# Performance work log

Hardware: AMD Instinct MI355X
Metric: run time of the kernel (lower is better)

## Reference

```python
import jax, jax.numpy as jnp
import numpy as np
from jax import lax

INPUT_SIZE = 64
HIDDEN_SIZE = 4096
OUTPUT_SIZE = 16
SEQ_LEN = 4096
SPECTRAL_RADIUS = 0.95
LEAKY_RATE = 0.9
INPUT_SCALING = 1.0
FEEDBACK_SCALING = 0.1
SPARSITY = 0.1


def setup_inputs() -> dict:
    key = jax.random.key(0)
    ks = jax.random.split(key, 7)
    X = jax.random.normal(ks[0], (SEQ_LEN, INPUT_SIZE), dtype=jnp.float32)
    W_in = jax.random.normal(ks[1], (HIDDEN_SIZE, INPUT_SIZE), dtype=jnp.float32) * INPUT_SCALING
    # sparse reservoir matrix, scaled so spectral radius ~ SPECTRAL_RADIUS
    dense = jax.random.normal(ks[2], (HIDDEN_SIZE, HIDDEN_SIZE), dtype=jnp.float32)
    mask = (jax.random.uniform(ks[3], (HIDDEN_SIZE, HIDDEN_SIZE)) < SPARSITY).astype(jnp.float32)
    # circular-law estimate of spectral radius for sparse gaussian: sqrt(density*N)
    scale = SPECTRAL_RADIUS / np.sqrt(SPARSITY * HIDDEN_SIZE)
    W_res = dense * mask * scale
    b = jax.random.normal(ks[4], (HIDDEN_SIZE,), dtype=jnp.float32)
    W_fb = jax.random.normal(ks[5], (HIDDEN_SIZE, OUTPUT_SIZE), dtype=jnp.float32) * FEEDBACK_SCALING
    W_out = jax.random.normal(ks[6], (OUTPUT_SIZE, HIDDEN_SIZE), dtype=jnp.float32) * 0.01
    return {"X": X, "W_in": W_in, "W_res": W_res, "b": b, "W_fb": W_fb, "W_out": W_out}


def reference(X, W_in, W_res, b, W_fb, W_out):
    """ESN with feedback + leaky integration; Force readout (inference: y = W_out @ s).
    Returns (results [T, O], outputs [T, H]) matching ESNForce.forward."""
    H = W_res.shape[0]
    O = W_out.shape[0]

    def step(carry, x_t):
        s, y = carry  # previous state [H], previous output [O]
        pre = W_in @ x_t + W_res @ s + b + W_fb @ y
        s_new = (1.0 - LEAKY_RATE) * s + LEAKY_RATE * jnp.tanh(pre)
        y_new = W_out @ s_new
        return (s_new, y_new), (y_new, s_new)

    init = (jnp.zeros((H,), dtype=X.dtype), jnp.zeros((O,), dtype=X.dtype))
    _, (results, outputs) = lax.scan(step, init, X)
    return results, outputs
```

## Files before the change

### kernel.cpp

```cpp
#include <hip/hip_runtime.h>
#include <cstdint>

#define NBLK 128
#define BLOCK 1024
#define ROWS 32
#define HDIM 4096
#define IDIM 64
#define ODIM 16
#define TSTEPS 4096
#define PAD 576
#define GMAX 18
#define LEAK 0.9f
#define SU 11
#define SUS 12
#define YU 8

typedef float f32x4 __attribute__((ext_vector_type(4)));

__global__ void init_ws(float* ws) {
    int i = blockIdx.x * blockDim.x + threadIdx.x;
    if (i < (2 * NBLK * SUS + 2 * NBLK * YU) * 4) ws[i] = 0.0f;
}

__global__ __launch_bounds__(BLOCK) void esn_kernel(
    const float* __restrict__ X,
    const float* __restrict__ Win,
    const float* __restrict__ Wres,
    const float* __restrict__ bvec,
    const float* __restrict__ Wfb,
    const float* __restrict__ Wout,
    float* __restrict__ out,
    float* __restrict__ sx,
    float* __restrict__ yx)
{
    __shared__ float          ell_val[ROWS][PAD];
    __shared__ unsigned short ell_idx[ROWS][PAD];
    __shared__ __align__(16) float s_lds[2][HDIM];
    __shared__ float          win_lds[ROWS][IDIM];
    __shared__ float          wfb_lds[ROWS][ODIM];
    __shared__ __align__(8)  float wout_lds[ROWS][ODIM];
    __shared__ float          b_lds[ROWS];
    __shared__ float          x_lds[2][IDIM];
    __shared__ float          y_lds[2][ODIM];
    __shared__ __align__(16) float snew_lds[ROWS];
    __shared__ unsigned       snflag[ROWS];
    __shared__ int            nnz_lds[ROWS];
    __shared__ int            rnds_lds[ROWS];
    __shared__ unsigned char  bankCnt[ROWS][32];
    __shared__ unsigned char  grpCnt[ROWS][GMAX];

    const int tid   = threadIdx.x;
    const int blk   = blockIdx.x;
    const int rbase = blk * ROWS;
    const int rowB  = tid >> 5;
    const int lB    = tid & 31;
    const int wv    = tid >> 6;
    const int ln    = tid & 63;

    for (int i = tid; i < ROWS * PAD; i += BLOCK) {
        ell_val[i / PAD][i % PAD] = 0.0f;
        ell_idx[i / PAD][i % PAD] = 0;
    }
    for (int i = tid; i < ROWS * 32; i += BLOCK) bankCnt[i >> 5][i & 31] = 0;
    for (int i = tid; i < ROWS * GMAX; i += BLOCK) grpCnt[i / GMAX][i % GMAX] = 0;
    if (tid < ROWS) snflag[tid] = 0u;

    {
        for (int rr = wv * 2; rr < wv * 2 + 2; ++rr) {
            const float* wrow = Wres + (size_t)(rbase + rr) * HDIM;
            int cnt = 0;
            for (int c0 = 0; c0 < HDIM; c0 += 64)
                cnt += __popcll(__ballot(wrow[c0 + ln] != 0.0f));
            if (ln == 0) {
                int nz = cnt < PAD ? cnt : PAD;
                nnz_lds[rr] = nz;
                int gu = (nz + 31) >> 5;
                if (gu < 1) gu = 1;
                if (gu > GMAX) gu = GMAX;
                rnds_lds[rr] = (gu + 1) >> 1;
            }
        }
    }
    __syncthreads();

    {
        if (ln == 0 || ln == 32) {
            const int row = wv * 2 + (ln >> 5);
            const int nz  = nnz_lds[row];
            int gu = (nz + 31) >> 5;
            if (gu < 1) gu = 1;
            if (gu > GMAX) gu = GMAX;
            const float* wrow = Wres + (size_t)(rbase + row) * HDIM;
            int placed = 0;
            for (int c = 0; c < HDIM && placed < nz; ++c) {
                const float w = wrow[c];
                if (w != 0.0f) {
                    const int b = c & 31;
                    const int r = bankCnt[row][b];
                    bankCnt[row][b] = (unsigned char)(r + 1);
                    int g = r % gu;
                    int p = grpCnt[row][g];
                    int guard = 0;
                    while (p >= 32 && guard < GMAX) {
                        g = (g + 1 == gu) ? 0 : g + 1;
                        p = grpCnt[row][g];
                        ++guard;
                    }
                    if (p >= 32) break;
                    grpCnt[row][g] = (unsigned char)(p + 1);
                    const int slot = ((g >> 1) << 6) + 2 * p + (g & 1);
                    ell_val[row][slot] = w;
                    ell_idx[row][slot] = (unsigned short)c;
                    ++placed;
                }
            }
        }
    }

    for (int i = tid; i < ROWS * IDIM; i += BLOCK)
        win_lds[i >> 6][i & 63] = Win[(size_t)(rbase + (i >> 6)) * IDIM + (i & 63)];
    for (int i = tid; i < ROWS * ODIM; i += BLOCK)
        wfb_lds[i >> 4][i & 15] = Wfb[(size_t)(rbase + (i >> 4)) * ODIM + (i & 15)];
    for (int i = tid; i < ROWS * ODIM; i += BLOCK)
        wout_lds[i >> 4][i & 15] = Wout[(size_t)(i & 15) * HDIM + rbase + (i >> 4)];
    if (tid < ROWS) b_lds[tid] = bvec[rbase + tid];

    for (int i = tid; i < HDIM; i += BLOCK) s_lds[0][i] = 0.0f;
    if (tid < ODIM) y_lds[0][tid] = 0.0f;
    if (tid >= 64 && tid < 128) x_lds[0][tid - 64] = X[tid - 64];
    __syncthreads();

    float* out_res = out;
    float* out_s   = out + (size_t)TSTEPS * ODIM;
    const int RB = rnds_lds[rowB];

    for (int t = 0; t < TSTEPS; ++t) {
        const unsigned tu = (unsigned)(t + 1);
        const float tagf = __uint_as_float(tu);
        const int cur = t & 1, nxt = cur ^ 1;

        {
            const float* sc = s_lds[cur];
            float a0 = 0.0f, a1 = 0.0f;
            for (int k = 0; k < RB; ++k) {
                const int e = (k << 6) + (lB << 1);
                const float2  v  = *(const float2*)&ell_val[rowB][e];
                const ushort2 ix = *(const ushort2*)&ell_idx[rowB][e];
                a0 += v.x * sc[ix.x];
                a1 += v.y * sc[ix.y];
            }
            float acc = a0 + a1;
            acc += win_lds[rowB][lB] * x_lds[cur][lB]
                 + win_lds[rowB][lB + 32] * x_lds[cur][lB + 32];
            if (lB < ODIM) acc += wfb_lds[rowB][lB] * y_lds[cur][lB];
            acc += __shfl_xor(acc, 16, 32);
            acc += __shfl_xor(acc, 8, 32);
            acc += __shfl_xor(acc, 4, 32);
            acc += __shfl_xor(acc, 2, 32);
            acc += __shfl_xor(acc, 1, 32);
            if (lB == 0) {
                const float pre = acc + b_lds[rowB];
                snew_lds[rowB] = (1.0f - LEAK) * sc[rbase + rowB] + LEAK * tanhf(pre);
                __hip_atomic_store(&snflag[rowB], tu, __ATOMIC_RELEASE,
                                   __HIP_MEMORY_SCOPE_WORKGROUP);
            }
        }

        if (wv == 0) {
            for (;;) {
                unsigned f = (ln < ROWS)
                    ? __hip_atomic_load(&snflag[ln], __ATOMIC_ACQUIRE, __HIP_MEMORY_SCOPE_WORKGROUP)
                    : tu;
                if (__all(f >= tu)) break;
            }
            if (ln >= 16 && ln < 16 + SU) {
                const int j  = ln - 16;
                const int b0 = 3 * j;
                const int b1 = (3 * j + 1 < 32) ? 3 * j + 1 : 31;
                const int b2 = (3 * j + 2 < 32) ? 3 * j + 2 : 31;
                f32x4 v;
                v.x = snew_lds[b0]; v.y = snew_lds[b1]; v.z = snew_lds[b2]; v.w = tagf;
                float* dst = sx + (((size_t)cur * NBLK + blk) * SUS + j) * 4;
                asm volatile("global_store_dwordx4 %0, %1, off sc0 sc1"
                             :: "v"(dst), "v"(v) : "memory");
            }
            if (ln < YU) {
                float a0 = 0.0f, a1 = 0.0f;
                #pragma unroll
                for (int r = 0; r < ROWS; ++r) {
                    const float2 w = *(const float2*)&wout_lds[r][2 * ln];
                    a0 += w.x * snew_lds[r];
                    a1 += w.y * snew_lds[r];
                }
                f32x4 v; v.x = a0; v.y = a1; v.z = tagf; v.w = 0.0f;
                float* dst = yx + (((size_t)cur * NBLK + blk) * YU + ln) * 4;
                asm volatile("global_store_dwordx4 %0, %1, off sc0 sc1"
                             :: "v"(dst), "v"(v) : "memory");
            }
            if (ln >= 32 && ln < 40) {
                const int j = ln - 32;
                *(f32x4*)(out_s + (size_t)t * HDIM + rbase + j * 4) =
                    *(const f32x4*)&snew_lds[j * 4];
            }
        } else if (wv == 1) {
            if (t + 1 < TSTEPS) x_lds[nxt][ln] = X[(size_t)(t + 1) * IDIM + ln];
            const int u  = ln & 7;
            const int pg = ln >> 3;
            const float* yb = yx + (size_t)cur * NBLK * YU * 4;
            f32x4 w0,w1,w2,w3,w4,w5,w6,w7,w8,w9,w10,w11,w12,w13,w14,w15;
            for (;;) {
                #define YL(i) asm volatile("global_load_dwordx4 %0, %1, off sc0 sc1" \
                    : "=v"(w##i) : "v"(yb + (((pg << 4) + i) * YU + u) * 4));
                YL(0) YL(1) YL(2) YL(3) YL(4) YL(5) YL(6) YL(7)
                YL(8) YL(9) YL(10) YL(11) YL(12) YL(13) YL(14) YL(15)
                #undef YL
                asm volatile("s_waitcnt vmcnt(0)" ::: "memory");
                __builtin_amdgcn_sched_barrier(0);
                bool ok = __float_as_uint(w0.z) == tu  && __float_as_uint(w1.z) == tu
                       && __float_as_uint(w2.z) == tu  && __float_as_uint(w3.z) == tu
                       && __float_as_uint(w4.z) == tu  && __float_as_uint(w5.z) == tu
                       && __float_as_uint(w6.z) == tu  && __float_as_uint(w7.z) == tu
                       && __float_as_uint(w8.z) == tu  && __float_as_uint(w9.z) == tu
                       && __float_as_uint(w10.z) == tu && __float_as_uint(w11.z) == tu
                       && __float_as_uint(w12.z) == tu && __float_as_uint(w13.z) == tu
                       && __float_as_uint(w14.z) == tu && __float_as_uint(w15.z) == tu;
                if (__all(ok)) break;
            }
            float acc0 = ((w0.x + w1.x) + (w2.x + w3.x)) + ((w4.x + w5.x) + (w6.x + w7.x))
                       + ((w8.x + w9.x) + (w10.x + w11.x)) + ((w12.x + w13.x) + (w14.x + w15.x));
            float acc1 = ((w0.y + w1.y) + (w2.y + w3.y)) + ((w4.y + w5.y) + (w6.y + w7.y))
                       + ((w8.y + w9.y) + (w10.y + w11.y)) + ((w12.y + w13.y) + (w14.y + w15.y));
            acc0 += __shfl_xor(acc0, 8);  acc1 += __shfl_xor(acc1, 8);
            acc0 += __shfl_xor(acc0, 16); acc1 += __shfl_xor(acc1, 16);
            acc0 += __shfl_xor(acc0, 32); acc1 += __shfl_xor(acc1, 32);
            if (ln < 8) {
                if (t + 1 < TSTEPS) { y_lds[nxt][2 * u] = acc0; y_lds[nxt][2 * u + 1] = acc1; }
                if (blk == 0) {
                    out_res[(size_t)t * ODIM + 2 * u]     = acc0;
                    out_res[(size_t)t * ODIM + 2 * u + 1] = acc1;
                }
            }
        } else {
            if (t + 1 < TSTEPS) {
                const int wi    = wv - 2;
                const int start = (wi < 2) ? wi * 10 : 20 + (wi - 2) * 9;
                const int count = (wi < 2) ? 10 : 9;
                const int U     = count * SU;
                const float* sb = sx + (size_t)cur * NBLK * SUS * 4;
                const int g0 = ln, g1 = ln + 64;
                const int p0 = g0 / SU, u0 = g0 - p0 * SU;
                const bool h1 = g1 < U;
                const int p1 = g1 / SU, u1 = g1 - p1 * SU;
                const float* a0p = sb + (((start + p0) * SUS) + u0) * 4;
                const float* a1p = sb + (((start + p1) * SUS) + u1) * 4;
                f32x4 v0, v1;
                for (;;) {
                    asm volatile("global_load_dwordx4 %0, %1, off sc0 sc1"
                                 : "=v"(v0) : "v"(a0p));
                    if (h1)
                        asm volatile("global_load_dwordx4 %0, %1, off sc0 sc1"
                                     : "=v"(v1) : "v"(a1p));
                    asm volatile("s_waitcnt vmcnt(0)" ::: "memory");
                    __builtin_amdgcn_sched_barrier(0);
                    bool ok = (__float_as_uint(v0.w) == tu) &&
                              (!h1 || __float_as_uint(v1.w) == tu);
                    if (__all(ok)) break;
                }
                float* sd = s_lds[nxt];
                {
                    const int c0 = (start + p0) * 32 + u0 * 3;
                    sd[c0] = v0.x; sd[c0 + 1] = v0.y;
                    if (u0 != SU - 1) sd[c0 + 2] = v0.z;
                }
                if (h1) {
                    const int c1 = (start + p1) * 32 + u1 * 3;
                    sd[c1] = v1.x; sd[c1 + 1] = v1.y;
                    if (u1 != SU - 1) sd[c1 + 2] = v1.z;
                }
            }
        }
        __syncthreads();
    }
}

extern "C" void kernel_launch(void* const* d_in, const int* in_sizes, int n_in,
                              void* d_out, int out_size, void* d_ws, size_t ws_size,
                              hipStream_t stream) {
    (void)in_sizes; (void)n_in; (void)out_size; (void)ws_size;
    const float* X    = (const float*)d_in[0];
    const float* Win  = (const float*)d_in[1];
    const float* Wres = (const float*)d_in[2];
    const float* b    = (const float*)d_in[3];
    const float* Wfb  = (const float*)d_in[4];
    const float* Wout = (const float*)d_in[5];
    float* out = (float*)d_out;
    float* sx  = (float*)d_ws;
    float* yx  = (float*)d_ws + 2 * NBLK * SUS * 4;

    const int words = (2 * NBLK * SUS + 2 * NBLK * YU) * 4;
    init_ws<<<(words + 255) / 256, 256, 0, stream>>>((float*)d_ws);
    esn_kernel<<<NBLK, BLOCK, 0, stream>>>(X, Win, Wres, b, Wfb, Wout, out, sx, yx);
}
```

Measured before the change: 21.43 ms.

## Publish state per wave directly to global and add intra-step barrier

Each wave now writes its two new state values plus a tag straight to the global exchange buffer, so the wave-0 spin on LDS flags is gone. A __syncthreads is inserted mid-step instead. The exchange packs 2 values per 16-byte packet (16 packets per block), and the LDS state copy uses a padded layout of 34 floats per block with remapped ELL indices. Consumer waves load up to 3 packets per lane. The change trades fewer serialized steps on the critical path for more global packets and an extra block barrier per timestep.

```diff
diff --git a/kernel.cpp b/kernel.cpp
--- a/kernel.cpp
+++ b/kernel.cpp
@@ -11,15 +11,15 @@
 #define PAD 576
 #define GMAX 18
 #define LEAK 0.9f
-#define SU 11
-#define SUS 12
+#define SUN 16
 #define YU 8
+#define SPAD 34
 
 typedef float f32x4 __attribute__((ext_vector_type(4)));
 
 __global__ void init_ws(float* ws) {
     int i = blockIdx.x * blockDim.x + threadIdx.x;
-    if (i < (2 * NBLK * SUS + 2 * NBLK * YU) * 4) ws[i] = 0.0f;
+    if (i < (2 * NBLK * SUN + 2 * NBLK * YU) * 4) ws[i] = 0.0f;
 }
 
 __global__ __launch_bounds__(BLOCK) void esn_kernel(
@@ -35,15 +35,14 @@
 {
     __shared__ float          ell_val[ROWS][PAD];
     __shared__ unsigned short ell_idx[ROWS][PAD];
-    __shared__ __align__(16) float s_lds[2][HDIM];
+    __shared__ __align__(16) float s_lds[2][NBLK*SPAD];
     __shared__ float          win_lds[ROWS][IDIM];
     __shared__ float          wfb_lds[ROWS][ODIM];
     __shared__ __align__(8)  float wout_lds[ROWS][ODIM];
     __shared__ float          b_lds[ROWS];
-    __shared__ float          x_lds[2][IDIM];
-    __shared__ float          y_lds[2][ODIM];
+    __shared__ float          x_lds[IDIM];
+    __shared__ float          y_lds[ODIM];
     __shared__ __align__(16) float snew_lds[ROWS];
-    __shared__ unsigned       snflag[ROWS];
     __shared__ int            nnz_lds[ROWS];
     __shared__ int            rnds_lds[ROWS];
     __shared__ unsigned char  bankCnt[ROWS][32];
@@ -63,56 +62,52 @@
     }
     for (int i = tid; i < ROWS * 32; i += BLOCK) bankCnt[i >> 5][i & 31] = 0;
     for (int i = tid; i < ROWS * GMAX; i += BLOCK) grpCnt[i / GMAX][i % GMAX] = 0;
-    if (tid < ROWS) snflag[tid] = 0u;
-
-    {
-        for (int rr = wv * 2; rr < wv * 2 + 2; ++rr) {
-            const float* wrow = Wres + (size_t)(rbase + rr) * HDIM;
-            int cnt = 0;
-            for (int c0 = 0; c0 < HDIM; c0 += 64)
-                cnt += __popcll(__ballot(wrow[c0 + ln] != 0.0f));
-            if (ln == 0) {
-                int nz = cnt < PAD ? cnt : PAD;
-                nnz_lds[rr] = nz;
-                int gu = (nz + 31) >> 5;
-                if (gu < 1) gu = 1;
-                if (gu > GMAX) gu = GMAX;
-                rnds_lds[rr] = (gu + 1) >> 1;
-            }
-        }
-    }
-    __syncthreads();
-
-    {
-        if (ln == 0 || ln == 32) {
-            const int row = wv * 2 + (ln >> 5);
-            const int nz  = nnz_lds[row];
+
+    for (int rr = wv * 2; rr < wv * 2 + 2; ++rr) {
+        const float* wrow = Wres + (size_t)(rbase + rr) * HDIM;
+        int cnt = 0;
+        for (int c0 = 0; c0 < HDIM; c0 += 64)
+            cnt += __popcll(__ballot(wrow[c0 + ln] != 0.0f));
+        if (ln == 0) {
+            int nz = cnt < PAD ? cnt : PAD;
+            nnz_lds[rr] = nz;
             int gu = (nz + 31) >> 5;
             if (gu < 1) gu = 1;
             if (gu > GMAX) gu = GMAX;
-            const float* wrow = Wres + (size_t)(rbase + row) * HDIM;
-            int placed = 0;
-            for (int c = 0; c < HDIM && placed < nz; ++c) {
-                const float w = wrow[c];
-                if (w != 0.0f) {
-                    const int b = c & 31;
-                    const int r = bankCnt[row][b];
-                    bankCnt[row][b] = (unsigned char)(r + 1);
-                    int g = r % gu;
-                    int p = grpCnt[row][g];
-                    int guard = 0;
-                    while (p >= 32 && guard < GMAX) {
-                        g = (g + 1 == gu) ? 0 : g + 1;
-                        p = grpCnt[row][g];
-                        ++guard;
-                    }
-                    if (p >= 32) break;
-                    grpCnt[row][g] = (unsigned char)(p + 1);
-                    const int slot = ((g >> 1) << 6) + 2 * p + (g & 1);
-                    ell_val[row][slot] = w;
-                    ell_idx[row][slot] = (unsigned short)c;
-                    ++placed;
-                }
+            rnds_lds[rr] = (gu + 1) >> 1;
+        }
+    }
+    __syncthreads();
+
+    if (ln == 0 || ln == 32) {
+        const int row = wv * 2 + (ln >> 5);
+        const int nz  = nnz_lds[row];
+        int gu = (nz + 31) >> 5;
+        if (gu < 1) gu = 1;
+        if (gu > GMAX) gu = GMAX;
+        const float* wrow = Wres + (size_t)(rbase + row) * HDIM;
+        int placed = 0;
+        for (int c = 0; c < HDIM && placed < nz; ++c) {
+            const float w = wrow[c];
+            if (w != 0.0f) {
+                const int pidx = c + 2 * (c >> 5);
+                const int b = pidx & 31;
+                const int r = bankCnt[row][b];
+                bankCnt[row][b] = (unsigned char)(r + 1);
+                int g = r % gu;
+                int p = grpCnt[row][g];
+                int guard = 0;
+                while (p >= 32 && guard < GMAX) {
+                    g = (g + 1 == gu) ? 0 : g + 1;
+                    p = grpCnt[row][g];
+                    ++guard;
+                }
+                if (p >= 32) break;
+                grpCnt[row][g] = (unsigned char)(p + 1);
+                const int slot = ((g >> 1) << 6) + 2 * p + (g & 1);
+                ell_val[row][slot] = w;
+                ell_idx[row][slot] = (unsigned short)pidx;
+                ++placed;
             }
         }
     }
@@ -125,9 +120,12 @@
         wout_lds[i >> 4][i & 15] = Wout[(size_t)(i & 15) * HDIM + rbase + (i >> 4)];
     if (tid < ROWS) b_lds[tid] = bvec[rbase + tid];
 
-    for (int i = tid; i < HDIM; i += BLOCK) s_lds[0][i] = 0.0f;
-    if (tid < ODIM) y_lds[0][tid] = 0.0f;
-    if (tid >= 64 && tid < 128) x_lds[0][tid - 64] = X[tid - 64];
+    {
+        float* sz = &s_lds[0][0];
+        for (int i = tid; i < 2 * NBLK * SPAD; i += BLOCK) sz[i] = 0.0f;
+    }
+    if (tid < ODIM) y_lds[tid] = 0.0f;
+    if (tid >= 64 && tid < 128) x_lds[tid - 64] = X[tid - 64];
     __syncthreads();
 
     float* out_res = out;
@@ -150,40 +148,32 @@
                 a1 += v.y * sc[ix.y];
             }
             float acc = a0 + a1;
-            acc += win_lds[rowB][lB] * x_lds[cur][lB]
-                 + win_lds[rowB][lB + 32] * x_lds[cur][lB + 32];
-            if (lB < ODIM) acc += wfb_lds[rowB][lB] * y_lds[cur][lB];
+            acc += win_lds[rowB][lB] * x_lds[lB] + win_lds[rowB][lB + 32] * x_lds[lB + 32];
+            if (lB < ODIM) acc += wfb_lds[rowB][lB] * y_lds[lB];
             acc += __shfl_xor(acc, 16, 32);
             acc += __shfl_xor(acc, 8, 32);
             acc += __shfl_xor(acc, 4, 32);
             acc += __shfl_xor(acc, 2, 32);
             acc += __shfl_xor(acc, 1, 32);
+            float sn = 0.0f;
             if (lB == 0) {
                 const float pre = acc + b_lds[rowB];
-                snew_lds[rowB] = (1.0f - LEAK) * sc[rbase + rowB] + LEAK * tanhf(pre);
-                __hip_atomic_store(&snflag[rowB], tu, __ATOMIC_RELEASE,
-                                   __HIP_MEMORY_SCOPE_WORKGROUP);
-            }
-        }
-
-        if (wv == 0) {
-            for (;;) {
-                unsigned f = (ln < ROWS)
-                    ? __hip_atomic_load(&snflag[ln], __ATOMIC_ACQUIRE, __HIP_MEMORY_SCOPE_WORKGROUP)
-                    : tu;
-                if (__all(f >= tu)) break;
-            }
-            if (ln >= 16 && ln < 16 + SU) {
-                const int j  = ln - 16;
-                const int b0 = 3 * j;
-                const int b1 = (3 * j + 1 < 32) ? 3 * j + 1 : 31;
-                const int b2 = (3 * j + 2 < 32) ? 3 * j + 2 : 31;
-                f32x4 v;
-                v.x = snew_lds[b0]; v.y = snew_lds[b1]; v.z = snew_lds[b2]; v.w = tagf;
-                float* dst = sx + (((size_t)cur * NBLK + blk) * SUS + j) * 4;
+                sn = (1.0f - LEAK) * sc[blk * SPAD + rowB] + LEAK * tanhf(pre);
+                snew_lds[rowB] = sn;
+            }
+            const float sn1 = __shfl(sn, 32);
+            if (ln == 0) {
+                f32x4 v; v.x = sn; v.y = sn1; v.z = 0.0f; v.w = tagf;
+                float* dst = sx + (((size_t)cur * NBLK + blk) * SUN + wv) * 4;
                 asm volatile("global_store_dwordx4 %0, %1, off sc0 sc1"
                              :: "v"(dst), "v"(v) : "memory");
-            }
+                float2 o2; o2.x = sn; o2.y = sn1;
+                *(float2*)(out_s + (size_t)t * HDIM + rbase + 2 * wv) = o2;
+            }
+        }
+        __syncthreads();
+
+        if (wv == 0) {
             if (ln < YU) {
                 float a0 = 0.0f, a1 = 0.0f;
                 #pragma unroll
@@ -197,13 +187,8 @@
                 asm volatile("global_store_dwordx4 %0, %1, off sc0 sc1"
                              :: "v"(dst), "v"(v) : "memory");
             }
-            if (ln >= 32 && ln < 40) {
-                const int j = ln - 32;
-                *(f32x4*)(out_s + (size_t)t * HDIM + rbase + j * 4) =
-                    *(const f32x4*)&snew_lds[j * 4];
-            }
         } else if (wv == 1) {
-            if (t + 1 < TSTEPS) x_lds[nxt][ln] = X[(size_t)(t + 1) * IDIM + ln];
+            if (t + 1 < TSTEPS) x_lds[ln] = X[(size_t)(t + 1) * IDIM + ln];
             const int u  = ln & 7;
             const int pg = ln >> 3;
             const float* yb = yx + (size_t)cur * NBLK * YU * 4;
@@ -234,7 +219,7 @@
             acc0 += __shfl_xor(acc0, 16); acc1 += __shfl_xor(acc1, 16);
             acc0 += __shfl_xor(acc0, 32); acc1 += __shfl_xor(acc1, 32);
             if (ln < 8) {
-                if (t + 1 < TSTEPS) { y_lds[nxt][2 * u] = acc0; y_lds[nxt][2 * u + 1] = acc1; }
+                if (t + 1 < TSTEPS) { y_lds[2 * u] = acc0; y_lds[2 * u + 1] = acc1; }
                 if (blk == 0) {
                     out_res[(size_t)t * ODIM + 2 * u]     = acc0;
                     out_res[(size_t)t * ODIM + 2 * u + 1] = acc1;
@@ -245,38 +230,39 @@
                 const int wi    = wv - 2;
                 const int start = (wi < 2) ? wi * 10 : 20 + (wi - 2) * 9;
                 const int count = (wi < 2) ? 10 : 9;
-                const int U     = count * SU;
-                const float* sb = sx + (size_t)cur * NBLK * SUS * 4;
-                const int g0 = ln, g1 = ln + 64;
-                const int p0 = g0 / SU, u0 = g0 - p0 * SU;
-                const bool h1 = g1 < U;
-                const int p1 = g1 / SU, u1 = g1 - p1 * SU;
-                const float* a0p = sb + (((start + p0) * SUS) + u0) * 4;
-                const float* a1p = sb + (((start + p1) * SUS) + u1) * 4;
-                f32x4 v0, v1;
+                const int U     = count * SUN;
+                const float* sb = sx + ((size_t)cur * NBLK + start) * SUN * 4;
+                const int g0 = ln, g1 = ln + 64, g2 = ln + 128;
+                const bool h1 = g1 < U, h2 = g2 < U;
+                f32x4 v0, v1, v2;
                 for (;;) {
                     asm volatile("global_load_dwordx4 %0, %1, off sc0 sc1"
-                                 : "=v"(v0) : "v"(a0p));
+                                 : "=v"(v0) : "v"(sb + (size_t)g0 * 4));
                     if (h1)
                         asm volatile("global_load_dwordx4 %0, %1, off sc0 sc1"
-                                     : "=v"(v1) : "v"(a1p));
+                                     : "=v"(v1) : "v"(sb + (size_t)g1 * 4));
+                    if (h2)
+                        asm volatile("global_load_dwordx4 %0, %1, off sc0 sc1"
+                                     : "=v"(v2) : "v"(sb + (size_t)g2 * 4));
                     asm volatile("s_waitcnt vmcnt(0)" ::: "memory");
                     __builtin_amdgcn_sched_barrier(0);
-                    bool ok = (__float_as_uint(v0.w) == tu) &&
-                              (!h1 || __float_as_uint(v1.w) == tu);
+                    bool ok = (__float_as_uint(v0.w) == tu)
+                           && (!h1 || __float_as_uint(v1.w) == tu)
+                           && (!h2 || __float_as_uint(v2.w) == tu);
                     if (__all(ok)) break;
                 }
                 float* sd = s_lds[nxt];
-                {
-                    const int c0 = (start + p0) * 32 + u0 * 3;
-                    sd[c0] = v0.x; sd[c0 + 1] = v0.y;
-                    if (u0 != SU - 1) sd[c0 + 2] = v0.z;
-                }
+                {   const int pp = start + (g0 >> 4), u = g0 & 15;
+                    float2 s2; s2.x = v0.x; s2.y = v0.y;
+                    *(float2*)&sd[pp * SPAD + 2 * u] = s2; }
                 if (h1) {
-                    const int c1 = (start + p1) * 32 + u1 * 3;
-                    sd[c1] = v1.x; sd[c1 + 1] = v1.y;
-                    if (u1 != SU - 1) sd[c1 + 2] = v1.z;
-                }
+                    const int pp = start + (g1 >> 4), u = g1 & 15;
+                    float2 s2; s2.x = v1.x; s2.y = v1.y;
+                    *(float2*)&sd[pp * SPAD + 2 * u] = s2; }
+                if (h2) {
+                    const int pp = start + (g2 >> 4), u = g2 & 15;
+                    float2 s2; s2.x = v2.x; s2.y = v2.y;
+                    *(float2*)&sd[pp * SPAD + 2 * u] = s2; }
             }
         }
         __syncthreads();
@@ -295,9 +281,9 @@
     const float* Wout = (const float*)d_in[5];
     float* out = (float*)d_out;
     float* sx  = (float*)d_ws;
-    float* yx  = (float*)d_ws + 2 * NBLK * SUS * 4;
-
-    const int words = (2 * NBLK * SUS + 2 * NBLK * YU) * 4;
+    float* yx  = (float*)d_ws + 2 * NBLK * SUN * 4;
+
+    const int words = (2 * NBLK * SUN + 2 * NBLK * YU) * 4;
     init_ws<<<(words + 255) / 256, 256, 0, stream>>>((float*)d_ws);
     esn_kernel<<<NBLK, BLOCK, 0, stream>>>(X, Win, Wres, b, Wfb, Wout, out, sx, yx);
 }
```

Result: faster. 19.46 ms (-9.2%).
